# Performance work log

Hardware: AMD Instinct MI355X
Metric: run time of the kernel (lower is better)

Reference implementation:

```python
import jax, jax.numpy as jnp
import numpy as np

C = 64  # channel dim fixed by Conv1D filters=64 and residual add

def setup_inputs() -> dict:
    key = jax.random.key(0)
    kF, kM, kN, kV = jax.random.split(key, 4)
    B, T = 8, 2048
    F = jax.random.normal(kF, (B, T, C), dtype=jnp.float32)
    # Conv1D(kernel_size=1, use_bias=False) == pointwise dense: weight [C_in, filters]
    scale = 1.0 / np.sqrt(C)
    W_M = jax.random.normal(kM, (C, C), dtype=jnp.float32) * scale
    W_N = jax.random.normal(kN, (C, C), dtype=jnp.float32) * scale
    W_V = jax.random.normal(kV, (C, C), dtype=jnp.float32) * scale
    return {"F": F, "W_M": W_M, "W_N": W_N, "W_V": W_V}

def reference(F, W_M, W_N, W_V):
    # 1x1 conv projections (pointwise matmul over channel dim)
    M = jnp.einsum('btc,cd->btd', F, W_M)  # Q
    N = jnp.einsum('btc,cd->btd', F, W_N)  # K
    V = jnp.einsum('btc,cd->btd', F, W_V)
    # correlation = Q @ K^T ; softmax over last axis (keras Softmax default)
    scores = jnp.einsum('bqd,bkd->bqk', M, N)  # [B, T, T]
    S = jax.nn.softmax(scores, axis=-1)
    out = jnp.einsum('bqk,bkd->bqd', S, V)
    return out + F  # residual
```

## Files before the change

### kernel.cpp

```cpp
#include <hip/hip_runtime.h>
#include <hip/hip_bf16.h>

#define B_ 8
#define T_ 2048
#define LOG2E 1.4426950408889634f

typedef _Float16 half8 __attribute__((ext_vector_type(8)));
typedef _Float16 half4 __attribute__((ext_vector_type(4)));
typedef float f32x4 __attribute__((ext_vector_type(4)));

#define MFMA16(A, Bv, Cv) __builtin_amdgcn_mfma_f32_16x16x32_f16((A), (Bv), (Cv), 0, 0, 0)

__device__ inline float xexp2(float x)
{
    float r;
    asm("v_exp_f32 %0, %1" : "=v"(r) : "v"(x));
    return r;
}

__global__ __launch_bounds__(256) void prepack_kernel(
    const float* __restrict__ WM, const float* __restrict__ WN,
    const float* __restrict__ WV, _Float16* __restrict__ Wp)
{
    const int idx = blockIdx.x * 256 + threadIdx.x;
    const int m = idx >> 12;
    const int r = idx & 4095;
    const int d = r >> 6;
    const int k = r & 63;
    const float* W = (m == 0) ? WM : (m == 1) ? WN : WV;
    Wp[m * 4096 + d * 64 + k] = (_Float16)W[k * 64 + d];
}

__global__ __launch_bounds__(256) void proj_kernel(
    const float* __restrict__ F, const _Float16* __restrict__ Wp,
    _Float16* __restrict__ Qh, _Float16* __restrict__ Kf,
    _Float16* __restrict__ Vf)
{
    const int lane = threadIdx.x & 63;
    const int dt   = threadIdx.x >> 6;
    const int ql = lane & 15;
    const int g  = lane >> 4;
    const int blk = blockIdx.x;
    const int b   = blk & 7;
    const int rt  = blk >> 3;
    const int rowbase = b * T_ + rt * 16;

    const float* fr = F + (size_t)(rowbase + ql) * 64;
    const f32x4 v00 = *(const f32x4*)(fr + 8 * g);
    const f32x4 v01 = *(const f32x4*)(fr + 8 * g + 4);
    const f32x4 v10 = *(const f32x4*)(fr + 32 + 8 * g);
    const f32x4 v11 = *(const f32x4*)(fr + 32 + 8 * g + 4);
    half8 af0, af1;
#pragma unroll
    for (int j = 0; j < 4; ++j) {
        af0[j]     = (_Float16)v00[j];
        af0[4 + j] = (_Float16)v01[j];
        af1[j]     = (_Float16)v10[j];
        af1[4 + j] = (_Float16)v11[j];
    }

    const half8* wq = (const half8*)(Wp);
    const half8* wk = (const half8*)(Wp + 4096);
    const half8* wv = (const half8*)(Wp + 8192);

    const int fi = (dt * 16 + ql) * 8;
    f32x4 z = {0.f, 0.f, 0.f, 0.f};
    f32x4 accQ = MFMA16(wq[fi + g], af0, z);
    accQ = MFMA16(wq[fi + 4 + g], af1, accQ);
    f32x4 accK = MFMA16(wk[fi + g], af0, z);
    accK = MFMA16(wk[fi + 4 + g], af1, accK);
    f32x4 accV = MFMA16(af0, wv[fi + g], z);
    accV = MFMA16(af1, wv[fi + 4 + g], accV);

    {
        half4 qs;
#pragma unroll
        for (int r = 0; r < 4; ++r) qs[r] = (_Float16)(accQ[r] * LOG2E);
        *(half4*)(Qh + (size_t)(rowbase + ql) * 64 + dt * 16 + 4 * g) = qs;
    }
    {
        half4 ks;
#pragma unroll
        for (int r = 0; r < 4; ++r) ks[r] = (_Float16)accK[r];
        const int d0 = dt * 16 + 4 * g;
        const int p  = ((d0 >> 5) << 2) | ((d0 >> 3) & 3);
        *(half4*)(Kf + (((size_t)b * 128 + rt) * 8 + p) * 128 + ql * 8 + (d0 & 7)) = ks;
    }
    {
        half4 vs;
#pragma unroll
        for (int r = 0; r < 4; ++r) vs[r] = (_Float16)accV[r];
        const int kt5 = rt >> 1;
        const int cp0 = 8 * g + 4 * (rt & 1);
        *(half4*)(Vf + ((((size_t)b * 64 + kt5) * 4 + dt) * 16 + ql) * 32 + cp0) = vs;
    }
}

#define PROC(qf0, qf1, a0, a1, a2, a3, mr, ls)                               \
    do {                                                                     \
        f32x4 s0 = {0.f, 0.f, 0.f, 0.f};                                     \
        f32x4 s1 = {0.f, 0.f, 0.f, 0.f};                                     \
        s0 = MFMA16(k0lo, qf0, s0);                                          \
        s0 = MFMA16(k0hi, qf1, s0);                                          \
        s1 = MFMA16(k1lo, qf0, s1);                                          \
        s1 = MFMA16(k1hi, qf1, s1);                                          \
        const float p0 = s0[0], p1 = s0[1], p2 = s0[2], p3 = s0[3];          \
        const float p4 = s1[0], p5 = s1[1], p6 = s1[2], p7 = s1[3];          \
        const float q0_ = fmaxf(fmaxf(p0, p1), p2);                          \
        const float q1_ = fmaxf(fmaxf(p3, p4), p5);                          \
        const float q2_ = fmaxf(fmaxf(p6, p7), q0_);                         \
        const float pm  = fmaxf(q1_, q2_);                                   \
        if (__any(pm - mr > 8.0f)) {                                         \
            float pmw = fmaxf(pm, __shfl_xor(pm, 16));                       \
            pmw = fmaxf(pmw, __shfl_xor(pmw, 32));                           \
            const float mnew = fmaxf(mr, pmw);                               \
            const float fac  = xexp2(mr - mnew);                             \
            mr = mnew;                                                       \
            ls *= fac;                                                       \
            const int lg = 4 * ((threadIdx.x & 63) >> 4);                    \
            const int lb = (threadIdx.x & 48);                               \
            const float f0 = __shfl(fac, lb | (lg + 0));                     \
            const float f1 = __shfl(fac, lb | (lg + 1));                     \
            const float f2 = __shfl(fac, lb | (lg + 2));                     \
            const float f3 = __shfl(fac, lb | (lg + 3));                     \
            a0[0] *= f0; a0[1] *= f1; a0[2] *= f2; a0[3] *= f3;              \
            a1[0] *= f0; a1[1] *= f1; a1[2] *= f2; a1[3] *= f3;              \
            a2[0] *= f0; a2[1] *= f1; a2[2] *= f2; a2[3] *= f3;              \
            a3[0] *= f0; a3[1] *= f1; a3[2] *= f2; a3[3] *= f3;              \
        }                                                                    \
        const float e0 = xexp2(p0 - mr), e1 = xexp2(p1 - mr);                \
        const float e2 = xexp2(p2 - mr), e3 = xexp2(p3 - mr);                \
        const float e4 = xexp2(p4 - mr), e5 = xexp2(p5 - mr);                \
        const float e6 = xexp2(p6 - mr), e7 = xexp2(p7 - mr);                \
        ls += ((e0 + e1) + (e2 + e3)) + ((e4 + e5) + (e6 + e7));             \
        half8 pav;                                                           \
        pav[0] = (_Float16)e0; pav[1] = (_Float16)e1;                        \
        pav[2] = (_Float16)e2; pav[3] = (_Float16)e3;                        \
        pav[4] = (_Float16)e4; pav[5] = (_Float16)e5;                        \
        pav[6] = (_Float16)e6; pav[7] = (_Float16)e7;                        \
        a0 = MFMA16(pav, v0, a0);                                            \
        a1 = MFMA16(pav, v1, a1);                                            \
        a2 = MFMA16(pav, v2, a2);                                            \
        a3 = MFMA16(pav, v3, a3);                                            \
    } while (0)

__global__ __launch_bounds__(256, 2) void attn_kernel(
    const _Float16* __restrict__ Qh, const _Float16* __restrict__ Kf,
    const _Float16* __restrict__ Vf, const float* __restrict__ F,
    float* __restrict__ out)
{
    __shared__ float Ol[4][32][68];
    __shared__ float Ml[4][32];
    __shared__ float Ll[4][32];

    const int lane = threadIdx.x & 63;
    const int wid  = threadIdx.x >> 6;
    const int blk  = blockIdx.x;
    const int b    = blk & 7;
    const int tile = blk >> 3;
    const int ql = lane & 15;
    const int g  = lane >> 4;

    const _Float16* Qbb = Qh + (size_t)b * T_ * 64;
    const half8* KfB = (const half8*)Kf + (size_t)b * 16384;
    const half8* VfB = (const half8*)Vf + (size_t)b * 16384;

    const int qb = tile * 32;
    const half8* qpA = (const half8*)(Qbb + (qb +      ql) * 64);
    const half8* qpB = (const half8*)(Qbb + (qb + 16 + ql) * 64);
    const half8 qA0 = qpA[g], qA1 = qpA[4 + g];
    const half8 qB0 = qpB[g], qB1 = qpB[4 + g];

    const f32x4 z4 = {0.f, 0.f, 0.f, 0.f};
    f32x4 aA0 = z4, aA1 = z4, aA2 = z4, aA3 = z4;
    f32x4 aB0 = z4, aB1 = z4, aB2 = z4, aB3 = z4;
    float mA = -1e30f, lsA = 0.f;
    float mB = -1e30f, lsB = 0.f;

    const int kb0 = wid << 9;
    const half8* kA = KfB + (size_t)(kb0 >> 4) * 128 + g * 16 + ql;
    const half8* vA = VfB + (size_t)(kb0 >> 5) * 256 + ql * 4 + g;

    half8 k0lo = kA[0];
    half8 k0hi = kA[64];
    half8 k1lo = kA[128];
    half8 k1hi = kA[192];
    half8 v0 = vA[0];
    half8 v1 = vA[64];
    half8 v2 = vA[128];
    half8 v3 = vA[192];

    for (int it = 0; it < 16; ++it) {
        half8 nk0lo, nk0hi, nk1lo, nk1hi, nv0, nv1, nv2, nv3;
        if (it < 15) {
            nk0lo = kA[256];
            nk0hi = kA[256 + 64];
            nk1lo = kA[256 + 128];
            nk1hi = kA[256 + 192];
            nv0 = vA[256];
            nv1 = vA[256 + 64];
            nv2 = vA[256 + 128];
            nv3 = vA[256 + 192];
        }

        PROC(qA0, qA1, aA0, aA1, aA2, aA3, mA, lsA);
        PROC(qB0, qB1, aB0, aB1, aB2, aB3, mB, lsB);

        if (it < 15) {
            k0lo = nk0lo; k0hi = nk0hi; k1lo = nk1lo; k1hi = nk1hi;
            v0 = nv0; v1 = nv1; v2 = nv2; v3 = nv3;
        }
        kA += 256;
        vA += 256;
    }

    lsA += __shfl_xor(lsA, 16); lsA += __shfl_xor(lsA, 32);
    lsB += __shfl_xor(lsB, 16); lsB += __shfl_xor(lsB, 32);

#pragma unroll
    for (int r = 0; r < 4; ++r) {
        Ol[wid][     4 * g + r][ 0 + ql] = aA0[r];
        Ol[wid][     4 * g + r][16 + ql] = aA1[r];
        Ol[wid][     4 * g + r][32 + ql] = aA2[r];
        Ol[wid][     4 * g + r][48 + ql] = aA3[r];
        Ol[wid][16 + 4 * g + r][ 0 + ql] = aB0[r];
        Ol[wid][16 + 4 * g + r][16 + ql] = aB1[r];
        Ol[wid][16 + 4 * g + r][32 + ql] = aB2[r];
        Ol[wid][16 + 4 * g + r][48 + ql] = aB3[r];
    }
    if (g == 0) {
        Ml[wid][     ql] = mA;  Ll[wid][     ql] = lsA;
        Ml[wid][16 + ql] = mB;  Ll[wid][16 + ql] = lsB;
    }
    __syncthreads();

    const int tid = threadIdx.x;
    const int qq  = tid >> 3;
    const int d0  = (tid & 7) * 8;

    float mm[4], lv[4];
#pragma unroll
    for (int s = 0; s < 4; ++s) {
        mm[s] = Ml[s][qq];
        lv[s] = Ll[s][qq];
    }
    const float ms = fmaxf(fmaxf(mm[0], mm[1]), fmaxf(mm[2], mm[3]));
    float lt = 0.f;
    f32x4 oa = {0.f, 0.f, 0.f, 0.f};
    f32x4 ob2 = {0.f, 0.f, 0.f, 0.f};
#pragma unroll
    for (int s = 0; s < 4; ++s) {
        const float sc = xexp2(mm[s] - ms);
        lt += lv[s] * sc;
        oa  += *(const f32x4*)(&Ol[s][qq][d0])     * sc;
        ob2 += *(const f32x4*)(&Ol[s][qq][d0 + 4]) * sc;
    }
    const float inv = 1.0f / lt;
    const size_t grow = (size_t)b * T_ + qb + qq;
    const f32x4 fr0 = *(const f32x4*)(F + grow * 64 + d0);
    const f32x4 fr1 = *(const f32x4*)(F + grow * 64 + d0 + 4);
    *(f32x4*)(out + grow * 64 + d0)     = oa * inv + fr0;
    *(f32x4*)(out + grow * 64 + d0 + 4) = ob2 * inv + fr1;
}

extern "C" void kernel_launch(void* const* d_in, const int* in_sizes, int n_in,
                              void* d_out, int out_size, void* d_ws, size_t ws_size,
                              hipStream_t stream)
{
    const float* F  = (const float*)d_in[0];
    const float* WM = (const float*)d_in[1];
    const float* WN = (const float*)d_in[2];
    const float* WV = (const float*)d_in[3];
    float* out = (float*)d_out;

    const size_t proj_bytes = (size_t)B_ * T_ * 64 * sizeof(_Float16);
    char* ws = (char*)d_ws;
    _Float16* Qh = (_Float16*)(ws);
    _Float16* Kf = (_Float16*)(ws + proj_bytes);
    _Float16* Vf = (_Float16*)(ws + 2 * proj_bytes);
    _Float16* Wp = (_Float16*)(ws + 3 * proj_bytes);

    hipLaunchKernelGGL(prepack_kernel, dim3(48), dim3(256), 0, stream,
                       WM, WN, WV, Wp);
    hipLaunchKernelGGL(proj_kernel, dim3(B_ * T_ / 16), dim3(256), 0, stream,
                       F, Wp, Qh, Kf, Vf);
    hipLaunchKernelGGL(attn_kernel, dim3(B_ * T_ / 32), dim3(256), 0, stream,
                       Qh, Kf, Vf, F, out);
}
```

Before: 32.22 us.

## Widen attention blocks to 64 queries over 8 waves, reusing K/V fragments

```diff
diff --git a/kernel.cpp b/kernel.cpp
--- a/kernel.cpp
+++ b/kernel.cpp
@@ -33,7 +33,7 @@
 
 __global__ __launch_bounds__(256) void proj_kernel(
     const float* __restrict__ F, const _Float16* __restrict__ Wp,
-    _Float16* __restrict__ Qh, _Float16* __restrict__ Kf,
+    _Float16* __restrict__ Qf, _Float16* __restrict__ Kf,
     _Float16* __restrict__ Vf)
 {
     const int lane = threadIdx.x & 63;
@@ -72,19 +72,20 @@
     f32x4 accV = MFMA16(af0, wv[fi + g], z);
     accV = MFMA16(af1, wv[fi + 4 + g], accV);
 
+    const int d0 = dt * 16 + 4 * g;
+    const int p  = ((d0 >> 5) << 2) | ((d0 >> 3) & 3);
+    const size_t tbase = (((size_t)b * 128 + rt) * 8 + p) * 128 + ql * 8 + (d0 & 7);
     {
         half4 qs;
 #pragma unroll
         for (int r = 0; r < 4; ++r) qs[r] = (_Float16)(accQ[r] * LOG2E);
-        *(half4*)(Qh + (size_t)(rowbase + ql) * 64 + dt * 16 + 4 * g) = qs;
+        *(half4*)(Qf + tbase) = qs;
     }
     {
         half4 ks;
 #pragma unroll
         for (int r = 0; r < 4; ++r) ks[r] = (_Float16)accK[r];
-        const int d0 = dt * 16 + 4 * g;
-        const int p  = ((d0 >> 5) << 2) | ((d0 >> 3) & 3);
-        *(half4*)(Kf + (((size_t)b * 128 + rt) * 8 + p) * 128 + ql * 8 + (d0 & 7)) = ks;
+        *(half4*)(Kf + tbase) = ks;
     }
     {
         half4 vs;
@@ -144,14 +145,14 @@
         a3 = MFMA16(pav, v3, a3);                                            \
     } while (0)
 
-__global__ __launch_bounds__(256, 2) void attn_kernel(
-    const _Float16* __restrict__ Qh, const _Float16* __restrict__ Kf,
+__global__ __launch_bounds__(512, 1) void attn_kernel(
+    const _Float16* __restrict__ Qf, const _Float16* __restrict__ Kf,
     const _Float16* __restrict__ Vf, const float* __restrict__ F,
     float* __restrict__ out)
 {
-    __shared__ float Ol[4][32][68];
-    __shared__ float Ml[4][32];
-    __shared__ float Ll[4][32];
+    __shared__ float Ol[8][64][68];
+    __shared__ float Ml[8][64];
+    __shared__ float Ll[8][64];
 
     const int lane = threadIdx.x & 63;
     const int wid  = threadIdx.x >> 6;
@@ -161,23 +162,30 @@
     const int ql = lane & 15;
     const int g  = lane >> 4;
 
-    const _Float16* Qbb = Qh + (size_t)b * T_ * 64;
+    const half8* QfB = (const half8*)Qf + (size_t)b * 16384;
     const half8* KfB = (const half8*)Kf + (size_t)b * 16384;
     const half8* VfB = (const half8*)Vf + (size_t)b * 16384;
 
-    const int qb = tile * 32;
-    const half8* qpA = (const half8*)(Qbb + (qb +      ql) * 64);
-    const half8* qpB = (const half8*)(Qbb + (qb + 16 + ql) * 64);
-    const half8 qA0 = qpA[g], qA1 = qpA[4 + g];
-    const half8 qB0 = qpB[g], qB1 = qpB[4 + g];
+    const half8* qtA = QfB + (size_t)(4 * tile + 0) * 128;
+    const half8* qtB = QfB + (size_t)(4 * tile + 1) * 128;
+    const half8* qtC = QfB + (size_t)(4 * tile + 2) * 128;
+    const half8* qtD = QfB + (size_t)(4 * tile + 3) * 128;
+    const half8 qA0 = qtA[g * 16 + ql], qA1 = qtA[(4 + g) * 16 + ql];
+    const half8 qB0 = qtB[g * 16 + ql], qB1 = qtB[(4 + g) * 16 + ql];
+    const half8 qC0 = qtC[g * 16 + ql], qC1 = qtC[(4 + g) * 16 + ql];
+    const half8 qD0 = qtD[g * 16 + ql], qD1 = qtD[(4 + g) * 16 + ql];
 
     const f32x4 z4 = {0.f, 0.f, 0.f, 0.f};
     f32x4 aA0 = z4, aA1 = z4, aA2 = z4, aA3 = z4;
     f32x4 aB0 = z4, aB1 = z4, aB2 = z4, aB3 = z4;
+    f32x4 aC0 = z4, aC1 = z4, aC2 = z4, aC3 = z4;
+    f32x4 aD0 = z4, aD1 = z4, aD2 = z4, aD3 = z4;
     float mA = -1e30f, lsA = 0.f;
     float mB = -1e30f, lsB = 0.f;
-
-    const int kb0 = wid << 9;
+    float mC = -1e30f, lsC = 0.f;
+    float mD = -1e30f, lsD = 0.f;
+
+    const int kb0 = wid << 8;
     const half8* kA = KfB + (size_t)(kb0 >> 4) * 128 + g * 16 + ql;
     const half8* vA = VfB + (size_t)(kb0 >> 5) * 256 + ql * 4 + g;
 
@@ -190,9 +198,9 @@
     half8 v2 = vA[128];
     half8 v3 = vA[192];
 
-    for (int it = 0; it < 16; ++it) {
+    for (int it = 0; it < 8; ++it) {
         half8 nk0lo, nk0hi, nk1lo, nk1hi, nv0, nv1, nv2, nv3;
-        if (it < 15) {
+        if (it < 7) {
             nk0lo = kA[256];
             nk0hi = kA[256 + 64];
             nk1lo = kA[256 + 128];
@@ -205,8 +213,10 @@
 
         PROC(qA0, qA1, aA0, aA1, aA2, aA3, mA, lsA);
         PROC(qB0, qB1, aB0, aB1, aB2, aB3, mB, lsB);
-
-        if (it < 15) {
+        PROC(qC0, qC1, aC0, aC1, aC2, aC3, mC, lsC);
+        PROC(qD0, qD1, aD0, aD1, aD2, aD3, mD, lsD);
+
+        if (it < 7) {
             k0lo = nk0lo; k0hi = nk0hi; k1lo = nk1lo; k1hi = nk1hi;
             v0 = nv0; v1 = nv1; v2 = nv2; v3 = nv3;
         }
@@ -216,6 +226,8 @@
 
     lsA += __shfl_xor(lsA, 16); lsA += __shfl_xor(lsA, 32);
     lsB += __shfl_xor(lsB, 16); lsB += __shfl_xor(lsB, 32);
+    lsC += __shfl_xor(lsC, 16); lsC += __shfl_xor(lsC, 32);
+    lsD += __shfl_xor(lsD, 16); lsD += __shfl_xor(lsD, 32);
 
 #pragma unroll
     for (int r = 0; r < 4; ++r) {
@@ -227,10 +239,20 @@
         Ol[wid][16 + 4 * g + r][16 + ql] = aB1[r];
         Ol[wid][16 + 4 * g + r][32 + ql] = aB2[r];
         Ol[wid][16 + 4 * g + r][48 + ql] = aB3[r];
+        Ol[wid][32 + 4 * g + r][ 0 + ql] = aC0[r];
+        Ol[wid][32 + 4 * g + r][16 + ql] = aC1[r];
+        Ol[wid][32 + 4 * g + r][32 + ql] = aC2[r];
+        Ol[wid][32 + 4 * g + r][48 + ql] = aC3[r];
+        Ol[wid][48 + 4 * g + r][ 0 + ql] = aD0[r];
+        Ol[wid][48 + 4 * g + r][16 + ql] = aD1[r];
+        Ol[wid][48 + 4 * g + r][32 + ql] = aD2[r];
+        Ol[wid][48 + 4 * g + r][48 + ql] = aD3[r];
     }
     if (g == 0) {
         Ml[wid][     ql] = mA;  Ll[wid][     ql] = lsA;
         Ml[wid][16 + ql] = mB;  Ll[wid][16 + ql] = lsB;
+        Ml[wid][32 + ql] = mC;  Ll[wid][32 + ql] = lsC;
+        Ml[wid][48 + ql] = mD;  Ll[wid][48 + ql] = lsD;
     }
     __syncthreads();
 
@@ -238,25 +260,27 @@
     const int qq  = tid >> 3;
     const int d0  = (tid & 7) * 8;
 
-    float mm[4], lv[4];
-#pragma unroll
-    for (int s = 0; s < 4; ++s) {
+    float mm[8], lv[8];
+#pragma unroll
+    for (int s = 0; s < 8; ++s) {
         mm[s] = Ml[s][qq];
         lv[s] = Ll[s][qq];
     }
-    const float ms = fmaxf(fmaxf(mm[0], mm[1]), fmaxf(mm[2], mm[3]));
+    float ms = mm[0];
+#pragma unroll
+    for (int s = 1; s < 8; ++s) ms = fmaxf(ms, mm[s]);
     float lt = 0.f;
     f32x4 oa = {0.f, 0.f, 0.f, 0.f};
     f32x4 ob2 = {0.f, 0.f, 0.f, 0.f};
 #pragma unroll
-    for (int s = 0; s < 4; ++s) {
+    for (int s = 0; s < 8; ++s) {
         const float sc = xexp2(mm[s] - ms);
         lt += lv[s] * sc;
         oa  += *(const f32x4*)(&Ol[s][qq][d0])     * sc;
         ob2 += *(const f32x4*)(&Ol[s][qq][d0 + 4]) * sc;
     }
     const float inv = 1.0f / lt;
-    const size_t grow = (size_t)b * T_ + qb + qq;
+    const size_t grow = (size_t)b * T_ + (tile << 6) + qq;
     const f32x4 fr0 = *(const f32x4*)(F + grow * 64 + d0);
     const f32x4 fr1 = *(const f32x4*)(F + grow * 64 + d0 + 4);
     *(f32x4*)(out + grow * 64 + d0)     = oa * inv + fr0;
@@ -275,7 +299,7 @@
 
     const size_t proj_bytes = (size_t)B_ * T_ * 64 * sizeof(_Float16);
     char* ws = (char*)d_ws;
-    _Float16* Qh = (_Float16*)(ws);
+    _Float16* Qf = (_Float16*)(ws);
     _Float16* Kf = (_Float16*)(ws + proj_bytes);
     _Float16* Vf = (_Float16*)(ws + 2 * proj_bytes);
     _Float16* Wp = (_Float16*)(ws + 3 * proj_bytes);
@@ -283,7 +307,7 @@
     hipLaunchKernelGGL(prepack_kernel, dim3(48), dim3(256), 0, stream,
                        WM, WN, WV, Wp);
     hipLaunchKernelGGL(proj_kernel, dim3(B_ * T_ / 16), dim3(256), 0, stream,
-                       F, Wp, Qh, Kf, Vf);
-    hipLaunchKernelGGL(attn_kernel, dim3(B_ * T_ / 32), dim3(256), 0, stream,
-                       Qh, Kf, Vf, F, out);
-}
+                       F, Wp, Qf, Kf, Vf);
+    hipLaunchKernelGGL(attn_kernel, dim3(B_ * T_ / 64), dim3(512), 0, stream,
+                       Qf, Kf, Vf, F, out);
+}
```

Result: no change. 32.43 us (+0.7%).
